# Kernel optimization log

Measured on AMD Instinct MI355X. Metric: run time of the kernel, lower is better.

## Reference

```python
import jax, jax.numpy as jnp
import numpy as np

DIM = 256; SEQ = 2048; WIN = 64; HEADS = 4; RANK = 32; LAYERS = 3; VOCAB = 32000
EPS = 1e-6

def _unit(v):
    # unit_normalize_values: project onto unit sphere along feature dim
    return v / jnp.maximum(jnp.linalg.norm(v, axis=-1, keepdims=True), EPS)

def _signed_softmax(s):
    # signed_softmax_state: sign(s) * softmax(|s|) over nodes
    return jnp.sign(s) * jax.nn.softmax(jnp.abs(s), axis=-1)

def setup_inputs() -> dict:
    key = jax.random.key(0)
    ks = jax.random.split(key, 10)
    d = DIM
    return {
        "input_ids": jax.random.randint(ks[0], (2, SEQ), 0, VOCAB, dtype=jnp.int32),
        "emb": 0.02 * jax.random.normal(ks[1], (VOCAB, d), jnp.float32),
        "pos_emb": 0.02 * jax.random.normal(ks[2], (SEQ, d), jnp.float32),
        "anchor_val": 0.02 * jax.random.normal(ks[3], (d,), jnp.float32),
        "anchor_state": jnp.zeros((), jnp.float32),
        "Ws": 0.02 * jax.random.normal(ks[4], (d,), jnp.float32),
        "bs": jnp.zeros((), jnp.float32),
        "U": 0.02 * jax.random.normal(ks[5], (LAYERS, d, HEADS, RANK), jnp.float32),
        "V": 0.02 * jax.random.normal(ks[6], (LAYERS, d, HEADS, RANK), jnp.float32),
        "W1": 0.02 * jax.random.normal(ks[7], (LAYERS, d, 2 * d), jnp.float32),
        "b1": jnp.zeros((LAYERS, 2 * d), jnp.float32),
        "W2": 0.02 * jax.random.normal(ks[8], (LAYERS, 2 * d, d), jnp.float32),
        "b2": jnp.zeros((LAYERS, d), jnp.float32),
    }

def _forward(emb, pos_emb, anchor_val, anchor_state, Ws, bs, U, V, W1, b1, W2, b2, input_ids):
    B, S = input_ids.shape
    tok = emb[input_ids] + pos_emb[None, :S]          # [B,S,D]
    state_src = tok                                    # state projected from pre-unit-norm values
    tok = _unit(tok)
    tstate = state_src @ Ws + bs                       # [B,S] scalar state per node
    val = jnp.concatenate([jnp.broadcast_to(_unit(anchor_val), (B, 1, DIM)), tok], axis=1)
    state = jnp.concatenate([jnp.broadcast_to(anchor_state, (B, 1)), tstate], axis=1)
    N = S + 1
    offs = jnp.arange(-WIN, WIN + 1)
    idx = jnp.arange(N)[:, None] + offs[None, :]       # [N,K]
    valid = (idx >= 0) & (idx < N)
    idxc = jnp.clip(idx, 0, N - 1)
    inv_sqrt_r = np.float32(1.0 / np.sqrt(RANK))
    for l in range(LAYERS):
        q = jnp.einsum('bnd,dhr->bnhr', val, U[l])
        k = jnp.einsum('bnd,dhr->bnhr', val, V[l])
        knb = k[:, idxc]                               # [B,N,K,H,R] window gather
        s = jnp.einsum('bnhr,bnkhr->bnkh', q, knb) * inv_sqrt_r
        s = s.max(axis=-1)                             # max head-aggregate [B,N,K]
        a = jnp.where(valid, jnp.abs(s), -jnp.inf)
        wgt = jnp.where(valid, jnp.sign(s) * jax.nn.softmax(a, axis=-1), 0.0)  # signed-abs-softmax edges
        dval = jnp.einsum('bnk,bnkd->bnd', wgt, val[:, idxc])
        dstate = jnp.sum(wgt * state[:, idxc], axis=-1)
        # apply_delta: residual + norm(identity) + unit-norm + touched-mask where
        updated = val + dval
        nv = _unit(updated)
        touched = jnp.max(jnp.abs(jax.lax.stop_gradient(dval)), axis=-1, keepdims=True) > 0
        val = jnp.where(touched, nv, updated)
        state = _signed_softmax(state + dstate)
        # residual feed-forward then re-unit-norm
        h = jax.nn.gelu(jnp.einsum('bnd,dh->bnh', val, W1[l]) + b1[l], approximate=False)
        val = _unit(val + jnp.einsum('bnh,hd->bnd', h, W2[l]) + b2[l])
    return state, val

def reference(input_ids, emb, pos_emb, anchor_val, anchor_state, Ws, bs, U, V, W1, b1, W2, b2):
    return _forward(emb, pos_emb, anchor_val, anchor_state, Ws, bs, U, V, W1, b1, W2, b2, input_ids)
```

## Files before the change

### kernel.cpp

```cpp
#include <hip/hip_runtime.h>
#include <hip/hip_bf16.h>
#include <math.h>

#define BB 2
#define SS 2048
#define NN 2049
#define MM (BB*NN)
#define DD 256
#define HR 128
#define NHEAD 4
#define WINW 64
#define DFF 512
#define EPSF 1e-6f
#define TB8 257

typedef __attribute__((ext_vector_type(8))) short bf16x8;
typedef __attribute__((ext_vector_type(4))) float f32x4;

__device__ __forceinline__ float wave_sum(float v) {
    v += __shfl_down(v, 32, 64); v += __shfl_down(v, 16, 64);
    v += __shfl_down(v, 8, 64);  v += __shfl_down(v, 4, 64);
    v += __shfl_down(v, 2, 64);  v += __shfl_down(v, 1, 64);
    return v;
}
__device__ __forceinline__ float wave_max(float v) {
    v = fmaxf(v, __shfl_down(v, 32, 64)); v = fmaxf(v, __shfl_down(v, 16, 64));
    v = fmaxf(v, __shfl_down(v, 8, 64));  v = fmaxf(v, __shfl_down(v, 4, 64));
    v = fmaxf(v, __shfl_down(v, 2, 64));  v = fmaxf(v, __shfl_down(v, 1, 64));
    return v;
}
__device__ __forceinline__ float block_sum(float v, float* red) {
    v = wave_sum(v);
    __syncthreads();
    if ((threadIdx.x & 63) == 0) red[threadIdx.x >> 6] = v;
    __syncthreads();
    return red[0] + red[1] + red[2] + red[3];
}
__device__ __forceinline__ float sgnf(float x) {
    return (x > 0.f) ? 1.f : ((x < 0.f) ? -1.f : 0.f);
}
__device__ __forceinline__ ushort f2b(float x) {
    __hip_bfloat16 h = __float2bfloat16(x);
    return *(ushort*)&h;
}
__device__ __forceinline__ float b2f(ushort u) {
    unsigned int v = ((unsigned int)u) << 16;
    return *(float*)&v;
}
__device__ __forceinline__ void split3(float x, ushort& h, ushort& m, ushort& l) {
    h = f2b(x);
    float r1 = x - b2f(h);
    m = f2b(r1);
    l = f2b(r1 - b2f(m));
}
__device__ __forceinline__ void pack_map(int e, int N, int& k, int& n) {
    int j = e & 7;
    int l = (e >> 3) & 63;
    int c = e >> 9;
    int ntiles = N >> 4;
    int kt = c / ntiles, nt = c - kt * ntiles;
    k = kt * 32 + ((l >> 4) << 3) + j;
    n = nt * 16 + (l & 15);
}
__device__ __forceinline__ void dma16(const ushort* g, ushort* lds) {
    __builtin_amdgcn_global_load_lds(
        (const __attribute__((address_space(1))) unsigned int*)g,
        (__attribute__((address_space(3))) unsigned int*)lds,
        16, 0, 0);
}

__global__ void pre_kernel(const int* __restrict__ ids,
                           const float* __restrict__ emb,
                           const float* __restrict__ pos,
                           const float* __restrict__ anchor_val,
                           const float* __restrict__ anchor_state,
                           const float* __restrict__ Ws,
                           const float* __restrict__ bs,
                           float* __restrict__ val,
                           ushort* __restrict__ v0, ushort* __restrict__ v1,
                           ushort* __restrict__ v2,
                           float* __restrict__ state,
                           const float* __restrict__ W1, const float* __restrict__ W2,
                           const float* __restrict__ U,  const float* __restrict__ V,
                           ushort* __restrict__ W1ph, ushort* __restrict__ W1pl,
                           ushort* __restrict__ W2ph, ushort* __restrict__ W2pl,
                           ushort* __restrict__ U0, ushort* __restrict__ U1,
                           ushort* __restrict__ U2,
                           ushort* __restrict__ V0, ushort* __restrict__ V1,
                           ushort* __restrict__ V2) {
    __shared__ float red[4];
    int bid = blockIdx.x;
    int t = threadIdx.x;
    if (bid < MM) {
        int b = bid / NN, n = bid % NN;
        float e;
        if (n == 0) {
            e = anchor_val[t];
        } else {
            int id = ids[b * SS + (n - 1)];
            e = emb[(size_t)id * DD + t] + pos[(size_t)(n - 1) * DD + t];
        }
        float ss = block_sum(e * e, red);
        float ts = block_sum(e * Ws[t], red);
        float rn = 1.f / fmaxf(sqrtf(ss), EPSF);
        float o = e * rn;
        size_t oi = (size_t)bid * DD + t;
        val[oi] = o;
        ushort h, m, lo;
        split3(o, h, m, lo);
        v0[oi] = h; v1[oi] = m; v2[oi] = lo;
        if (t == 0) state[bid] = (n == 0) ? anchor_state[0] : (ts + bs[0]);
        return;
    }
    int idx = (bid - MM) * 256 + t;
    int l = idx / 327680;
    int r = idx - l * 327680;
    if (l >= 3) return;
    int k, n;
    if (r < 131072) {
        int e = r;
        pack_map(e, 512, k, n);
        float s = W1[(size_t)l * 131072 + (size_t)k * 512 + n];
        ushort h = f2b(s);
        W1ph[(size_t)l * 131072 + e] = h;
        W1pl[(size_t)l * 131072 + e] = f2b(s - b2f(h));
    } else if (r < 262144) {
        int e = r - 131072;
        pack_map(e, 256, k, n);
        float s = W2[(size_t)l * 131072 + (size_t)k * 256 + n];
        ushort h = f2b(s);
        W2ph[(size_t)l * 131072 + e] = h;
        W2pl[(size_t)l * 131072 + e] = f2b(s - b2f(h));
    } else if (r < 294912) {
        int e = r - 262144;
        pack_map(e, 128, k, n);
        ushort h, m, lo;
        split3(U[(size_t)l * 32768 + (size_t)k * 128 + n], h, m, lo);
        U0[(size_t)l * 32768 + e] = h;
        U1[(size_t)l * 32768 + e] = m;
        U2[(size_t)l * 32768 + e] = lo;
    } else {
        int e = r - 294912;
        pack_map(e, 128, k, n);
        ushort h, m, lo;
        split3(V[(size_t)l * 32768 + (size_t)k * 128 + n], h, m, lo);
        V0[(size_t)l * 32768 + e] = h;
        V1[(size_t)l * 32768 + e] = m;
        V2[(size_t)l * 32768 + e] = lo;
    }
}

__global__ __launch_bounds__(256, 2)
void proj_kernel(const ushort* __restrict__ X0, const ushort* __restrict__ X1,
                 const ushort* __restrict__ X2,
                 const ushort* __restrict__ U0, const ushort* __restrict__ U1,
                 const ushort* __restrict__ U2,
                 const ushort* __restrict__ V0, const ushort* __restrict__ V1,
                 const ushort* __restrict__ V2,
                 ushort* __restrict__ q0, ushort* __restrict__ q1,
                 ushort* __restrict__ q2,
                 ushort* __restrict__ k0, ushort* __restrict__ k1,
                 ushort* __restrict__ k2) {
    __shared__ __align__(16) ushort stage[2][24 * 512];
    int t = threadIdx.x;
    int w = t >> 6, l = t & 63;
    int lm = l & 15, quad = l >> 4;
    int m0 = blockIdx.x * 16;
    bool isQ = (blockIdx.y == 0);
    const ushort* P[3];
    P[0] = isQ ? U0 : V0;
    P[1] = isQ ? U1 : V1;
    P[2] = isQ ? U2 : V2;
    int row0 = m0 + lm; if (row0 > MM - 1) row0 = MM - 1;
    const ushort* xb0 = X0 + (size_t)row0 * DD + quad * 8;
    const ushort* xb1 = X1 + (size_t)row0 * DD + quad * 8;
    const ushort* xb2 = X2 + (size_t)row0 * DD + quad * 8;

    bf16x8 a0[2], a1[2], a2[2];
    a0[0] = *(const bf16x8*)(xb0);
    a1[0] = *(const bf16x8*)(xb1);
    a2[0] = *(const bf16x8*)(xb2);
    #pragma unroll
    for (int i = 0; i < 6; i++) {
        int c = w * 6 + i;
        int p = c >> 3, ntl = c & 7;
        dma16(P[p] + ((size_t)ntl * 64 + l) * 8,
              &stage[0][c * 512 + l * 8]);
    }
    asm volatile("" ::: "memory");

    f32x4 acc[2];
    acc[0] = (f32x4)(0.f); acc[1] = (f32x4)(0.f);
    #pragma unroll
    for (int kt = 0; kt < 8; kt++) {
        int cur = kt & 1;
        if (kt < 7) {
            a0[cur ^ 1] = *(const bf16x8*)(xb0 + (kt + 1) * 32);
            a1[cur ^ 1] = *(const bf16x8*)(xb1 + (kt + 1) * 32);
            a2[cur ^ 1] = *(const bf16x8*)(xb2 + (kt + 1) * 32);
            #pragma unroll
            for (int i = 0; i < 6; i++) {
                int c = w * 6 + i;
                int p = c >> 3, ntl = c & 7;
                dma16(P[p] + ((size_t)((kt + 1) * 8 + ntl) * 64 + l) * 8,
                      &stage[cur ^ 1][c * 512 + l * 8]);
            }
            asm volatile("s_waitcnt vmcnt(9)" ::: "memory");
        } else {
            asm volatile("s_waitcnt vmcnt(0)" ::: "memory");
        }
        __builtin_amdgcn_s_barrier();
        #pragma unroll
        for (int jj = 0; jj < 2; jj++) {
            int ntl = w * 2 + jj;
            bf16x8 b0 = *(const bf16x8*)&stage[cur][(0 * 8 + ntl) * 512 + l * 8];
            bf16x8 b1 = *(const bf16x8*)&stage[cur][(1 * 8 + ntl) * 512 + l * 8];
            bf16x8 b2 = *(const bf16x8*)&stage[cur][(2 * 8 + ntl) * 512 + l * 8];
            acc[jj] = __builtin_amdgcn_mfma_f32_16x16x32_bf16(a0[cur], b0, acc[jj], 0, 0, 0);
            acc[jj] = __builtin_amdgcn_mfma_f32_16x16x32_bf16(a0[cur], b1, acc[jj], 0, 0, 0);
            acc[jj] = __builtin_amdgcn_mfma_f32_16x16x32_bf16(a1[cur], b0, acc[jj], 0, 0, 0);
            acc[jj] = __builtin_amdgcn_mfma_f32_16x16x32_bf16(a1[cur], b1, acc[jj], 0, 0, 0);
            acc[jj] = __builtin_amdgcn_mfma_f32_16x16x32_bf16(a0[cur], b2, acc[jj], 0, 0, 0);
            acc[jj] = __builtin_amdgcn_mfma_f32_16x16x32_bf16(a2[cur], b0, acc[jj], 0, 0, 0);
        }
        __builtin_amdgcn_s_barrier();
    }
    ushort* o0 = isQ ? q0 : k0;
    ushort* o1 = isQ ? q1 : k1;
    ushort* o2 = isQ ? q2 : k2;
    #pragma unroll
    for (int jj = 0; jj < 2; jj++) {
        int n = (w * 2 + jj) * 16 + lm;
        #pragma unroll
        for (int r = 0; r < 4; r++) {
            int tok = m0 + quad * 4 + r;
            if (tok < MM) {
                ushort h, m, lo;
                split3(acc[jj][r], h, m, lo);
                size_t oi = (size_t)tok * HR + n;
                o0[oi] = h; o1[oi] = m; o2[oi] = lo;
            }
        }
    }
}

__global__ __launch_bounds__(256, 2)
void attn_kernel(const float* __restrict__ val_in,
                 const float* __restrict__ state_in,
                 const ushort* __restrict__ q0, const ushort* __restrict__ q1,
                 const ushort* __restrict__ q2,
                 const ushort* __restrict__ k0, const ushort* __restrict__ k1,
                 const ushort* __restrict__ k2,
                 float* __restrict__ val_out,
                 ushort* __restrict__ vbH, ushort* __restrict__ vbM,
                 float* __restrict__ dstate_out) {
    __shared__ float sc4[NHEAD][8][148];
    __shared__ float wgt2[144][12];
    __shared__ float redS[8][4];
    __shared__ float redM[8][4];

    int b = blockIdx.x / TB8;
    int n0 = (blockIdx.x % TB8) * 8;
    int t = threadIdx.x;
    int w = t >> 6, l = t & 63;
    int lm = l & 15, quad = l >> 4;

    {
        int qrow = n0 + (lm & 7);
        if (qrow > NN - 1) qrow = NN - 1;
        size_t qa = ((size_t)(b * NN + qrow)) * HR + w * 32 + quad * 8;
        bf16x8 a0 = *(const bf16x8*)(q0 + qa);
        bf16x8 a1 = *(const bf16x8*)(q1 + qa);
        bf16x8 a2 = *(const bf16x8*)(q2 + qa);
        bf16x8 kf0[9], kf1[9], kf2[9];
        #pragma unroll
        for (int jt = 0; jt < 9; jt++) {
            int j = n0 - 64 + jt * 16 + lm;
            j = (j < 0) ? 0 : ((j > NN - 1) ? NN - 1 : j);
            size_t ka = ((size_t)(b * NN + j)) * HR + w * 32 + quad * 8;
            kf0[jt] = *(const bf16x8*)(k0 + ka);
            kf1[jt] = *(const bf16x8*)(k1 + ka);
            kf2[jt] = *(const bf16x8*)(k2 + ka);
        }
        #pragma unroll
        for (int jt = 0; jt < 9; jt++) {
            f32x4 acc = (f32x4)(0.f);
            acc = __builtin_amdgcn_mfma_f32_16x16x32_bf16(a0, kf0[jt], acc, 0, 0, 0);
            acc = __builtin_amdgcn_mfma_f32_16x16x32_bf16(a0, kf1[jt], acc, 0, 0, 0);
            acc = __builtin_amdgcn_mfma_f32_16x16x32_bf16(a1, kf0[jt], acc, 0, 0, 0);
            acc = __builtin_amdgcn_mfma_f32_16x16x32_bf16(a1, kf1[jt], acc, 0, 0, 0);
            acc = __builtin_amdgcn_mfma_f32_16x16x32_bf16(a0, kf2[jt], acc, 0, 0, 0);
            acc = __builtin_amdgcn_mfma_f32_16x16x32_bf16(a2, kf0[jt], acc, 0, 0, 0);
            if (quad < 2) {
                #pragma unroll
                for (int r = 0; r < 4; r++)
                    sc4[w][quad * 4 + r][jt * 16 + lm] = acc[r];
            }
        }
    }
    __syncthreads();

    {
        int m = t >> 5, p = t & 31;
        int n = n0 + m;
        bool tokv = (n < NN);
        float sv[5]; bool vv[5];
        float mx = -INFINITY;
        #pragma unroll
        for (int i = 0; i < 5; i++) {
            int tap = p + 32 * i;
            bool inb = (tap < 144);
            int tapc = inb ? tap : 0;
            int j = n0 - 64 + tapc;
            float s0 = sc4[0][m][tapc], s1 = sc4[1][m][tapc];
            float s2 = sc4[2][m][tapc], s3 = sc4[3][m][tapc];
            float s = fmaxf(fmaxf(s0, s1), fmaxf(s2, s3)) * 0.17677669529663687f;
            bool v = inb && tokv && (tap >= m) && (tap <= m + 128) && (j >= 0) && (j < NN);
            sv[i] = s; vv[i] = v;
            if (v) mx = fmaxf(mx, fabsf(s));
        }
        for (int off = 16; off > 0; off >>= 1) mx = fmaxf(mx, __shfl_xor(mx, off, 64));
        float ee[5];
        float sum = 0.f;
        #pragma unroll
        for (int i = 0; i < 5; i++) {
            ee[i] = vv[i] ? expf(fabsf(sv[i]) - mx) : 0.f;
            sum += ee[i];
        }
        for (int off = 16; off > 0; off >>= 1) sum += __shfl_xor(sum, off, 64);
        float inv = (sum > 0.f) ? 1.f / sum : 0.f;
        float ds = 0.f;
        #pragma unroll
        for (int i = 0; i < 5; i++) {
            int tap = p + 32 * i;
            if (tap < 144) {
                float wg = vv[i] ? sgnf(sv[i]) * ee[i] * inv : 0.f;
                wgt2[tap][m] = wg;
                if (vv[i]) ds += wg * state_in[b * NN + (n0 - 64 + tap)];
            }
        }
        for (int off = 16; off > 0; off >>= 1) ds += __shfl_xor(ds, off, 64);
        if (p == 0 && tokv) dstate_out[b * NN + n] = ds;
    }
    __syncthreads();

    {
        int d = (t >> 2) * 4;
        int tg = t & 3;
        int tok0 = tg * 2, tok1 = tg * 2 + 1;
        int jlo = (n0 >= 64) ? 0 : (64 - n0);
        int jhi = NN - 1 - n0 + 64; if (jhi > 135) jhi = 135;
        const float* vbase = val_in + ((size_t)(b * NN + n0 - 64)) * DD + d;
        f32x4 acc0 = (f32x4)(0.f), acc1 = (f32x4)(0.f);
        int jj = jlo;
        for (; jj + 3 <= jhi; jj += 4) {
            f32x4 v0 = *(const f32x4*)(vbase + (size_t)(jj + 0) * DD);
            f32x4 v1 = *(const f32x4*)(vbase + (size_t)(jj + 1) * DD);
            f32x4 v2 = *(const f32x4*)(vbase + (size_t)(jj + 2) * DD);
            f32x4 v3 = *(const f32x4*)(vbase + (size_t)(jj + 3) * DD);
            float wa0 = wgt2[jj + 0][tok0], wa1 = wgt2[jj + 0][tok1];
            float wb0 = wgt2[jj + 1][tok0], wb1 = wgt2[jj + 1][tok1];
            float wc0 = wgt2[jj + 2][tok0], wc1 = wgt2[jj + 2][tok1];
            float wd0 = wgt2[jj + 3][tok0], wd1 = wgt2[jj + 3][tok1];
            #pragma unroll
            for (int c = 0; c < 4; c++) {
                acc0[c] += v0[c] * wa0 + v1[c] * wb0 + v2[c] * wc0 + v3[c] * wd0;
                acc1[c] += v0[c] * wa1 + v1[c] * wb1 + v2[c] * wc1 + v3[c] * wd1;
            }
        }
        for (; jj <= jhi; jj++) {
            f32x4 v = *(const f32x4*)(vbase + (size_t)jj * DD);
            float w0 = wgt2[jj][tok0], w1 = wgt2[jj][tok1];
            #pragma unroll
            for (int c = 0; c < 4; c++) {
                acc0[c] += v[c] * w0;
                acc1[c] += v[c] * w1;
            }
        }
        f32x4 u[2]; f32x4 ac[2]; ac[0] = acc0; ac[1] = acc1;
        #pragma unroll
        for (int ti = 0; ti < 2; ti++) {
            int tok = tg * 2 + ti;
            int n = n0 + tok;
            f32x4 vold = (f32x4)(0.f);
            if (n < NN) vold = *(const f32x4*)(val_in + ((size_t)(b * NN + n)) * DD + d);
            u[ti] = vold + ac[ti];
            float s = u[ti][0]*u[ti][0] + u[ti][1]*u[ti][1] + u[ti][2]*u[ti][2] + u[ti][3]*u[ti][3];
            float mb = fmaxf(fmaxf(fabsf(ac[ti][0]), fabsf(ac[ti][1])),
                             fmaxf(fabsf(ac[ti][2]), fabsf(ac[ti][3])));
            for (int off = 4; off <= 32; off <<= 1) {
                s += __shfl_xor(s, off, 64);
                mb = fmaxf(mb, __shfl_xor(mb, off, 64));
            }
            if ((l >> 2) == 0) { redS[tok][w] = s; redM[tok][w] = mb; }
        }
        __syncthreads();
        #pragma unroll
        for (int ti = 0; ti < 2; ti++) {
            int tok = tg * 2 + ti;
            int n = n0 + tok;
            if (n < NN) {
                float ss = redS[tok][0] + redS[tok][1] + redS[tok][2] + redS[tok][3];
                float mab = fmaxf(fmaxf(redM[tok][0], redM[tok][1]),
                                  fmaxf(redM[tok][2], redM[tok][3]));
                float rn = 1.f / fmaxf(sqrtf(ss), EPSF);
                f32x4 o = u[ti];
                if (mab > 0.f) { o[0] *= rn; o[1] *= rn; o[2] *= rn; o[3] *= rn; }
                size_t oi = ((size_t)(b * NN + n)) * DD + d;
                *(f32x4*)(val_out + oi) = o;
                ushort4 hv, mv;
                {
                    ushort h0 = f2b(o[0]); hv.x = h0; mv.x = f2b(o[0] - b2f(h0));
                    ushort h1 = f2b(o[1]); hv.y = h1; mv.y = f2b(o[1] - b2f(h1));
                    ushort h2 = f2b(o[2]); hv.z = h2; mv.z = f2b(o[2] - b2f(h2));
                    ushort h3 = f2b(o[3]); hv.w = h3; mv.w = f2b(o[3] - b2f(h3));
                }
                *(ushort4*)(vbH + oi) = hv;
                *(ushort4*)(vbM + oi) = mv;
            }
        }
    }
}

__global__ __launch_bounds__(256, 2)
void ffn1_kernel(const ushort* __restrict__ XbH, const ushort* __restrict__ XbM,
                 const ushort* __restrict__ W1h, const ushort* __restrict__ W1l,
                 const float*  __restrict__ b1,
                 ushort* __restrict__ Hh, ushort* __restrict__ Hl,
                 const float* __restrict__ state_in, const float* __restrict__ dstate,
                 float* __restrict__ state_out) {
    __shared__ __align__(16) ushort stage[2][32 * 512];
    int t = threadIdx.x;

    if (blockIdx.x == 257) {
        float* red = (float*)&stage[0][0];
        int b = blockIdx.y;
        float lmax = -INFINITY;
        for (int n = t; n < NN; n += 256) {
            float x = state_in[b * NN + n] + dstate[b * NN + n];
            lmax = fmaxf(lmax, fabsf(x));
        }
        lmax = wave_max(lmax);
        if ((t & 63) == 0) red[t >> 6] = lmax;
        __syncthreads();
        float m = fmaxf(fmaxf(red[0], red[1]), fmaxf(red[2], red[3]));
        float lsum = 0.f;
        for (int n = t; n < NN; n += 256)
            lsum += expf(fabsf(state_in[b * NN + n] + dstate[b * NN + n]) - m);
        lsum = wave_sum(lsum);
        __syncthreads();
        if ((t & 63) == 0) red[4 + (t >> 6)] = lsum;
        __syncthreads();
        float inv = 1.f / (red[4] + red[5] + red[6] + red[7]);
        for (int n = t; n < NN; n += 256) {
            float x = state_in[b * NN + n] + dstate[b * NN + n];
            state_out[b * NN + n] = sgnf(x) * expf(fabsf(x) - m) * inv;
        }
        return;
    }

    int w = t >> 6, l = t & 63;
    int lm = l & 15, quad = l >> 4;
    int m0 = blockIdx.x * 16;
    int nh = blockIdx.y;
    int row0 = m0 + lm; if (row0 > MM - 1) row0 = MM - 1;
    const ushort* xh = XbH + (size_t)row0 * DD + quad * 8;
    const ushort* xm = XbM + (size_t)row0 * DD + quad * 8;

    bf16x8 ah[2], am[2];
    ah[0] = *(const bf16x8*)(xh);
    am[0] = *(const bf16x8*)(xm);
    #pragma unroll
    for (int i = 0; i < 8; i++) {
        int c = w * 8 + i;
        int p = c >> 4, ntl = c & 15;
        const ushort* src = (p ? W1l : W1h) + ((size_t)(nh * 16 + ntl) * 64 + l) * 8;
        dma16(src, &stage[0][c * 512 + l * 8]);
    }
    asm volatile("" ::: "memory");

    f32x4 acc[4];
    #pragma unroll
    for (int jj = 0; jj < 4; jj++) acc[jj] = (f32x4)(0.f);

    #pragma unroll
    for (int kt = 0; kt < 8; kt++) {
        int cur = kt & 1;
        if (kt < 7) {
            ah[cur ^ 1] = *(const bf16x8*)(xh + (kt + 1) * 32);
            am[cur ^ 1] = *(const bf16x8*)(xm + (kt + 1) * 32);
            #pragma unroll
            for (int i = 0; i < 8; i++) {
                int c = w * 8 + i;
                int p = c >> 4, ntl = c & 15;
                const ushort* src = (p ? W1l : W1h) +
                    ((size_t)((kt + 1) * 32 + nh * 16 + ntl) * 64 + l) * 8;
                dma16(src, &stage[cur ^ 1][c * 512 + l * 8]);
            }
            asm volatile("s_waitcnt vmcnt(10)" ::: "memory");
        } else {
            asm volatile("s_waitcnt vmcnt(0)" ::: "memory");
        }
        __builtin_amdgcn_s_barrier();
        #pragma unroll
        for (int jj = 0; jj < 4; jj++) {
            int ntl = w * 4 + jj;
            bf16x8 bh = *(const bf16x8*)&stage[cur][ntl * 512 + l * 8];
            bf16x8 bl = *(const bf16x8*)&stage[cur][(16 + ntl) * 512 + l * 8];
            acc[jj] = __builtin_amdgcn_mfma_f32_16x16x32_bf16(ah[cur], bh, acc[jj], 0, 0, 0);
            acc[jj] = __builtin_amdgcn_mfma_f32_16x16x32_bf16(am[cur], bh, acc[jj], 0, 0, 0);
            acc[jj] = __builtin_amdgcn_mfma_f32_16x16x32_bf16(ah[cur], bl, acc[jj], 0, 0, 0);
        }
        __builtin_amdgcn_s_barrier();
    }
    #pragma unroll
    for (int jj = 0; jj < 4; jj++) {
        int gn = nh * 256 + (w * 4 + jj) * 16 + lm;
        float bb = b1[gn];
        #pragma unroll
        for (int r = 0; r < 4; r++) {
            int tok = m0 + quad * 4 + r;
            if (tok < MM) {
                float x = acc[jj][r] + bb;
                float g = 0.5f * x * (1.f + erff(x * 0.70710678118654752f));
                ushort gh = f2b(g);
                size_t oi = (size_t)tok * DFF + gn;
                Hh[oi] = gh;
                Hl[oi] = f2b(g - b2f(gh));
            }
        }
    }
}

__global__ __launch_bounds__(256, 2)
void ffn2_kernel(const ushort* __restrict__ Hh, const ushort* __restrict__ Hl,
                 const float*  __restrict__ Xf,
                 const ushort* __restrict__ W2h, const ushort* __restrict__ W2l,
                 const float*  __restrict__ b2,
                 float* __restrict__ Yb) {
    __shared__ __align__(16) ushort stage[2][16 * 512];
    int t = threadIdx.x;
    int w = t >> 6, l = t & 63;
    int lm = l & 15, quad = l >> 4;
    int m0 = blockIdx.x * 16;
    int nh = blockIdx.y;
    int row0 = m0 + lm; if (row0 > MM - 1) row0 = MM - 1;
    const ushort* xh = Hh + (size_t)row0 * DFF + quad * 8;
    const ushort* xl = Hl + (size_t)row0 * DFF + quad * 8;

    bf16x8 ah[2], al[2];
    ah[0] = *(const bf16x8*)(xh);
    al[0] = *(const bf16x8*)(xl);
    #pragma unroll
    for (int i = 0; i < 4; i++) {
        int c = w * 4 + i;
        int p = c >> 3, ntl = c & 7;
        const ushort* src = (p ? W2l : W2h) + ((size_t)(nh * 8 + ntl) * 64 + l) * 8;
        dma16(src, &stage[0][c * 512 + l * 8]);
    }
    asm volatile("" ::: "memory");

    f32x4 acc[2];
    acc[0] = (f32x4)(0.f); acc[1] = (f32x4)(0.f);

    #pragma unroll
    for (int kt = 0; kt < 16; kt++) {
        int cur = kt & 1;
        if (kt < 15) {
            ah[cur ^ 1] = *(const bf16x8*)(xh + (kt + 1) * 32);
            al[cur ^ 1] = *(const bf16x8*)(xl + (kt + 1) * 32);
            #pragma unroll
            for (int i = 0; i < 4; i++) {
                int c = w * 4 + i;
                int p = c >> 3, ntl = c & 7;
                const ushort* src = (p ? W2l : W2h) +
                    ((size_t)((kt + 1) * 16 + nh * 8 + ntl) * 64 + l) * 8;
                dma16(src, &stage[cur ^ 1][c * 512 + l * 8]);
            }
            asm volatile("s_waitcnt vmcnt(6)" ::: "memory");
        } else {
            asm volatile("s_waitcnt vmcnt(0)" ::: "memory");
        }
        __builtin_amdgcn_s_barrier();
        #pragma unroll
        for (int jj = 0; jj < 2; jj++) {
            int ntl = w * 2 + jj;
            bf16x8 bh = *(const bf16x8*)&stage[cur][ntl * 512 + l * 8];
            bf16x8 bl = *(const bf16x8*)&stage[cur][(8 + ntl) * 512 + l * 8];
            acc[jj] = __builtin_amdgcn_mfma_f32_16x16x32_bf16(ah[cur], bh, acc[jj], 0, 0, 0);
            acc[jj] = __builtin_amdgcn_mfma_f32_16x16x32_bf16(al[cur], bh, acc[jj], 0, 0, 0);
            acc[jj] = __builtin_amdgcn_mfma_f32_16x16x32_bf16(ah[cur], bl, acc[jj], 0, 0, 0);
        }
        __builtin_amdgcn_s_barrier();
    }
    #pragma unroll
    for (int jj = 0; jj < 2; jj++) {
        int gn = nh * 128 + (w * 2 + jj) * 16 + lm;
        float bb = b2[gn];
        #pragma unroll
        for (int r = 0; r < 4; r++) {
            int tok = m0 + quad * 4 + r;
            if (tok < MM) {
                size_t oi = (size_t)tok * DD + gn;
                Yb[oi] = Xf[oi] + acc[jj][r] + bb;
            }
        }
    }
}

__global__ void ffn3_kernel(const float* __restrict__ Yb,
                            float* __restrict__ val_out,
                            ushort* __restrict__ o0, ushort* __restrict__ o1,
                            ushort* __restrict__ o2) {
    int t = threadIdx.x;
    int w = t >> 6, l = t & 63;
    int row = blockIdx.x * 4 + w;
    if (row >= MM) return;
    f32x4 y = *(const f32x4*)(Yb + (size_t)row * DD + l * 4);
    float s = y[0]*y[0] + y[1]*y[1] + y[2]*y[2] + y[3]*y[3];
    #pragma unroll
    for (int off = 1; off < 64; off <<= 1) s += __shfl_xor(s, off, 64);
    float rn = 1.f / fmaxf(sqrtf(s), EPSF);
    f32x4 o;
    o[0] = y[0] * rn; o[1] = y[1] * rn; o[2] = y[2] * rn; o[3] = y[3] * rn;
    size_t oi = (size_t)row * DD + l * 4;
    *(f32x4*)(val_out + oi) = o;
    ushort4 h4, m4, l4;
    ushort hh, mm, ll;
    split3(o[0], hh, mm, ll); h4.x = hh; m4.x = mm; l4.x = ll;
    split3(o[1], hh, mm, ll); h4.y = hh; m4.y = mm; l4.y = ll;
    split3(o[2], hh, mm, ll); h4.z = hh; m4.z = mm; l4.z = ll;
    split3(o[3], hh, mm, ll); h4.w = hh; m4.w = mm; l4.w = ll;
    *(ushort4*)(o0 + oi) = h4;
    *(ushort4*)(o1 + oi) = m4;
    *(ushort4*)(o2 + oi) = l4;
}

extern "C" void kernel_launch(void* const* d_in, const int* in_sizes, int n_in,
                              void* d_out, int out_size, void* d_ws, size_t ws_size,
                              hipStream_t stream) {
    const int*   ids          = (const int*)d_in[0];
    const float* emb          = (const float*)d_in[1];
    const float* pos          = (const float*)d_in[2];
    const float* anchor_val   = (const float*)d_in[3];
    const float* anchor_state = (const float*)d_in[4];
    const float* Ws           = (const float*)d_in[5];
    const float* bs           = (const float*)d_in[6];
    const float* U            = (const float*)d_in[7];
    const float* V            = (const float*)d_in[8];
    const float* W1           = (const float*)d_in[9];
    const float* b1           = (const float*)d_in[10];
    const float* W2           = (const float*)d_in[11];
    const float* b2           = (const float*)d_in[12];
    float* out = (float*)d_out;

    ushort* p = (ushort*)d_ws;
    ushort* vA0 = p; p += (size_t)MM * DD;
    ushort* vA1 = p; p += (size_t)MM * DD;
    ushort* vA2 = p; p += (size_t)MM * DD;
    ushort* vB0 = p; p += (size_t)MM * DD;
    ushort* vB1 = p; p += (size_t)MM * DD;
    ushort* q0b = p; p += (size_t)MM * HR;
    ushort* q1b = p; p += (size_t)MM * HR;
    ushort* q2b = p; p += (size_t)MM * HR;
    ushort* k0b = p; p += (size_t)MM * HR;
    ushort* k1b = p; p += (size_t)MM * HR;
    ushort* k2b = p; p += (size_t)MM * HR;
    ushort* Hh  = p; p += (size_t)MM * DFF;
    ushort* Hl  = p; p += (size_t)MM * DFF;
    ushort* W1ph = p; p += 3 * 131072;
    ushort* W1pl = p; p += 3 * 131072;
    ushort* W2ph = p; p += 3 * 131072;
    ushort* W2pl = p; p += 3 * 131072;
    ushort* U0p = p; p += 3 * 32768;
    ushort* U1p = p; p += 3 * 32768;
    ushort* U2p = p; p += 3 * 32768;
    ushort* V0p = p; p += 3 * 32768;
    ushort* V1p = p; p += 3 * 32768;
    ushort* V2p = p; p += 3 * 32768;
    float* f = (float*)p;
    float* valA = f; f += (size_t)MM * DD;
    float* valB = f; f += (size_t)MM * DD;
    float* st0  = f; f += MM;
    float* st1  = f; f += MM;
    float* dst  = f; f += MM;
    float* Yb   = valA;

    pre_kernel<<<MM + 3840, 256, 0, stream>>>(ids, emb, pos, anchor_val, anchor_state,
                                              Ws, bs, valA, vA0, vA1, vA2, st0,
                                              W1, W2, U, V,
                                              W1ph, W1pl, W2ph, W2pl,
                                              U0p, U1p, U2p, V0p, V1p, V2p);
    float* s_in = st0;
    float* s_out = st1;
    for (int l = 0; l < 3; l++) {
        proj_kernel<<<dim3(257, 2), 256, 0, stream>>>(
            vA0, vA1, vA2,
            U0p + (size_t)l * 32768, U1p + (size_t)l * 32768, U2p + (size_t)l * 32768,
            V0p + (size_t)l * 32768, V1p + (size_t)l * 32768, V2p + (size_t)l * 32768,
            q0b, q1b, q2b, k0b, k1b, k2b);
        attn_kernel<<<BB * TB8, 256, 0, stream>>>(valA, s_in,
                                                  q0b, q1b, q2b, k0b, k1b, k2b,
                                                  valB, vB0, vB1, dst);
        ffn1_kernel<<<dim3(258, 2), 256, 0, stream>>>(
            vB0, vB1,
            W1ph + (size_t)l * 131072, W1pl + (size_t)l * 131072, b1 + (size_t)l * DFF,
            Hh, Hl,
            s_in, dst, (l == 2) ? out : s_out);
        ffn2_kernel<<<dim3(257, 2), 256, 0, stream>>>(
            Hh, Hl, valB,
            W2ph + (size_t)l * 131072, W2pl + (size_t)l * 131072, b2 + (size_t)l * DD,
            Yb);
        ffn3_kernel<<<(MM + 3) / 4, 256, 0, stream>>>(
            Yb, (l == 2) ? (out + MM) : valA, vA0, vA1, vA2);
        float* tmp = s_in; s_in = s_out; s_out = tmp;
    }
}
```

Measured before the change: 357.8 us.

## Fuse final unit-norm and bf16 split into projection kernel, drop ffn3 launches

The per-layer ffn3 kernel, which normalized the FFN output and wrote three bf16 split planes, is removed. The projection kernel now reads fp32 values directly, optionally unit-normalizes each row, writes the normalized fp32 value back (Q blocks only), and builds the three bf16 planes in a swizzled LDS buffer for the MFMA loop. Only the last layer runs a standalone normalization kernel. This saves two kernel launches and the global round trip of the split planes, at the cost of more LDS and duplicated normalization work across the Q and K blocks.

```diff
diff --git a/kernel.cpp b/kernel.cpp
--- a/kernel.cpp
+++ b/kernel.cpp
@@ -77,8 +77,6 @@
                            const float* __restrict__ Ws,
                            const float* __restrict__ bs,
                            float* __restrict__ val,
-                           ushort* __restrict__ v0, ushort* __restrict__ v1,
-                           ushort* __restrict__ v2,
                            float* __restrict__ state,
                            const float* __restrict__ W1, const float* __restrict__ W2,
                            const float* __restrict__ U,  const float* __restrict__ V,
@@ -104,11 +102,7 @@
         float ts = block_sum(e * Ws[t], red);
         float rn = 1.f / fmaxf(sqrtf(ss), EPSF);
         float o = e * rn;
-        size_t oi = (size_t)bid * DD + t;
-        val[oi] = o;
-        ushort h, m, lo;
-        split3(o, h, m, lo);
-        v0[oi] = h; v1[oi] = m; v2[oi] = lo;
+        val[(size_t)bid * DD + t] = o;
         if (t == 0) state[bid] = (n == 0) ? anchor_state[0] : (ts + bs[0]);
         return;
     }
@@ -151,8 +145,7 @@
 }
 
 __global__ __launch_bounds__(256, 2)
-void proj_kernel(const ushort* __restrict__ X0, const ushort* __restrict__ X1,
-                 const ushort* __restrict__ X2,
+void proj_kernel(const float* __restrict__ Xin,
                  const ushort* __restrict__ U0, const ushort* __restrict__ U1,
                  const ushort* __restrict__ U2,
                  const ushort* __restrict__ V0, const ushort* __restrict__ V1,
@@ -160,8 +153,10 @@
                  ushort* __restrict__ q0, ushort* __restrict__ q1,
                  ushort* __restrict__ q2,
                  ushort* __restrict__ k0, ushort* __restrict__ k1,
-                 ushort* __restrict__ k2) {
+                 ushort* __restrict__ k2,
+                 float* __restrict__ valG, int donorm) {
     __shared__ __align__(16) ushort stage[2][24 * 512];
+    __shared__ __align__(16) ushort pln[3][16 * 256];
     int t = threadIdx.x;
     int w = t >> 6, l = t & 63;
     int lm = l & 15, quad = l >> 4;
@@ -171,15 +166,7 @@
     P[0] = isQ ? U0 : V0;
     P[1] = isQ ? U1 : V1;
     P[2] = isQ ? U2 : V2;
-    int row0 = m0 + lm; if (row0 > MM - 1) row0 = MM - 1;
-    const ushort* xb0 = X0 + (size_t)row0 * DD + quad * 8;
-    const ushort* xb1 = X1 + (size_t)row0 * DD + quad * 8;
-    const ushort* xb2 = X2 + (size_t)row0 * DD + quad * 8;
-
-    bf16x8 a0[2], a1[2], a2[2];
-    a0[0] = *(const bf16x8*)(xb0);
-    a1[0] = *(const bf16x8*)(xb1);
-    a2[0] = *(const bf16x8*)(xb2);
+
     #pragma unroll
     for (int i = 0; i < 6; i++) {
         int c = w * 6 + i;
@@ -189,15 +176,38 @@
     }
     asm volatile("" ::: "memory");
 
+    #pragma unroll
+    for (int rr = 0; rr < 4; rr++) {
+        int row = w * 4 + rr;
+        int tok = m0 + row; if (tok > MM - 1) tok = MM - 1;
+        f32x4 x = *(const f32x4*)(Xin + (size_t)tok * DD + l * 4);
+        if (donorm) {
+            float s = x[0]*x[0] + x[1]*x[1] + x[2]*x[2] + x[3]*x[3];
+            #pragma unroll
+            for (int off = 1; off < 64; off <<= 1) s += __shfl_xor(s, off, 64);
+            float rn = 1.f / fmaxf(sqrtf(s), EPSF);
+            x[0] *= rn; x[1] *= rn; x[2] *= rn; x[3] *= rn;
+            if (isQ) *(f32x4*)(valG + (size_t)tok * DD + l * 4) = x;
+        }
+        ushort4 h4, m4, l4;
+        ushort hh, mm, ll;
+        split3(x[0], hh, mm, ll); h4.x = hh; m4.x = mm; l4.x = ll;
+        split3(x[1], hh, mm, ll); h4.y = hh; m4.y = mm; l4.y = ll;
+        split3(x[2], hh, mm, ll); h4.z = hh; m4.z = mm; l4.z = ll;
+        split3(x[3], hh, mm, ll); h4.w = hh; m4.w = mm; l4.w = ll;
+        unsigned byte = ((unsigned)(row * 512 + l * 8)) ^ ((unsigned)((row & 7) << 4));
+        *(ushort4*)((char*)&pln[0][0] + byte) = h4;
+        *(ushort4*)((char*)&pln[1][0] + byte) = m4;
+        *(ushort4*)((char*)&pln[2][0] + byte) = l4;
+    }
+    __syncthreads();
+
     f32x4 acc[2];
     acc[0] = (f32x4)(0.f); acc[1] = (f32x4)(0.f);
     #pragma unroll
     for (int kt = 0; kt < 8; kt++) {
         int cur = kt & 1;
         if (kt < 7) {
-            a0[cur ^ 1] = *(const bf16x8*)(xb0 + (kt + 1) * 32);
-            a1[cur ^ 1] = *(const bf16x8*)(xb1 + (kt + 1) * 32);
-            a2[cur ^ 1] = *(const bf16x8*)(xb2 + (kt + 1) * 32);
             #pragma unroll
             for (int i = 0; i < 6; i++) {
                 int c = w * 6 + i;
@@ -205,23 +215,28 @@
                 dma16(P[p] + ((size_t)((kt + 1) * 8 + ntl) * 64 + l) * 8,
                       &stage[cur ^ 1][c * 512 + l * 8]);
             }
-            asm volatile("s_waitcnt vmcnt(9)" ::: "memory");
+            asm volatile("s_waitcnt vmcnt(6)" ::: "memory");
         } else {
             asm volatile("s_waitcnt vmcnt(0)" ::: "memory");
         }
         __builtin_amdgcn_s_barrier();
+        unsigned abyte = ((unsigned)(lm * 512 + kt * 64 + quad * 16)) ^
+                         ((unsigned)((lm & 7) << 4));
+        bf16x8 a0 = *(const bf16x8*)((char*)&pln[0][0] + abyte);
+        bf16x8 a1 = *(const bf16x8*)((char*)&pln[1][0] + abyte);
+        bf16x8 a2 = *(const bf16x8*)((char*)&pln[2][0] + abyte);
         #pragma unroll
         for (int jj = 0; jj < 2; jj++) {
             int ntl = w * 2 + jj;
             bf16x8 b0 = *(const bf16x8*)&stage[cur][(0 * 8 + ntl) * 512 + l * 8];
             bf16x8 b1 = *(const bf16x8*)&stage[cur][(1 * 8 + ntl) * 512 + l * 8];
             bf16x8 b2 = *(const bf16x8*)&stage[cur][(2 * 8 + ntl) * 512 + l * 8];
-            acc[jj] = __builtin_amdgcn_mfma_f32_16x16x32_bf16(a0[cur], b0, acc[jj], 0, 0, 0);
-            acc[jj] = __builtin_amdgcn_mfma_f32_16x16x32_bf16(a0[cur], b1, acc[jj], 0, 0, 0);
-            acc[jj] = __builtin_amdgcn_mfma_f32_16x16x32_bf16(a1[cur], b0, acc[jj], 0, 0, 0);
-            acc[jj] = __builtin_amdgcn_mfma_f32_16x16x32_bf16(a1[cur], b1, acc[jj], 0, 0, 0);
-            acc[jj] = __builtin_amdgcn_mfma_f32_16x16x32_bf16(a0[cur], b2, acc[jj], 0, 0, 0);
-            acc[jj] = __builtin_amdgcn_mfma_f32_16x16x32_bf16(a2[cur], b0, acc[jj], 0, 0, 0);
+            acc[jj] = __builtin_amdgcn_mfma_f32_16x16x32_bf16(a0, b0, acc[jj], 0, 0, 0);
+            acc[jj] = __builtin_amdgcn_mfma_f32_16x16x32_bf16(a0, b1, acc[jj], 0, 0, 0);
+            acc[jj] = __builtin_amdgcn_mfma_f32_16x16x32_bf16(a1, b0, acc[jj], 0, 0, 0);
+            acc[jj] = __builtin_amdgcn_mfma_f32_16x16x32_bf16(a1, b1, acc[jj], 0, 0, 0);
+            acc[jj] = __builtin_amdgcn_mfma_f32_16x16x32_bf16(a0, b2, acc[jj], 0, 0, 0);
+            acc[jj] = __builtin_amdgcn_mfma_f32_16x16x32_bf16(a2, b0, acc[jj], 0, 0, 0);
         }
         __builtin_amdgcn_s_barrier();
     }
@@ -608,10 +623,8 @@
     }
 }
 
-__global__ void ffn3_kernel(const float* __restrict__ Yb,
-                            float* __restrict__ val_out,
-                            ushort* __restrict__ o0, ushort* __restrict__ o1,
-                            ushort* __restrict__ o2) {
+__global__ void ffn3f_kernel(const float* __restrict__ Yb,
+                             float* __restrict__ val_out) {
     int t = threadIdx.x;
     int w = t >> 6, l = t & 63;
     int row = blockIdx.x * 4 + w;
@@ -623,17 +636,7 @@
     float rn = 1.f / fmaxf(sqrtf(s), EPSF);
     f32x4 o;
     o[0] = y[0] * rn; o[1] = y[1] * rn; o[2] = y[2] * rn; o[3] = y[3] * rn;
-    size_t oi = (size_t)row * DD + l * 4;
-    *(f32x4*)(val_out + oi) = o;
-    ushort4 h4, m4, l4;
-    ushort hh, mm, ll;
-    split3(o[0], hh, mm, ll); h4.x = hh; m4.x = mm; l4.x = ll;
-    split3(o[1], hh, mm, ll); h4.y = hh; m4.y = mm; l4.y = ll;
-    split3(o[2], hh, mm, ll); h4.z = hh; m4.z = mm; l4.z = ll;
-    split3(o[3], hh, mm, ll); h4.w = hh; m4.w = mm; l4.w = ll;
-    *(ushort4*)(o0 + oi) = h4;
-    *(ushort4*)(o1 + oi) = m4;
-    *(ushort4*)(o2 + oi) = l4;
+    *(f32x4*)(val_out + (size_t)row * DD + l * 4) = o;
 }
 
 extern "C" void kernel_launch(void* const* d_in, const int* in_sizes, int n_in,
@@ -655,9 +658,6 @@
     float* out = (float*)d_out;
 
     ushort* p = (ushort*)d_ws;
-    ushort* vA0 = p; p += (size_t)MM * DD;
-    ushort* vA1 = p; p += (size_t)MM * DD;
-    ushort* vA2 = p; p += (size_t)MM * DD;
     ushort* vB0 = p; p += (size_t)MM * DD;
     ushort* vB1 = p; p += (size_t)MM * DD;
     ushort* q0b = p; p += (size_t)MM * HR;
@@ -681,24 +681,26 @@
     float* f = (float*)p;
     float* valA = f; f += (size_t)MM * DD;
     float* valB = f; f += (size_t)MM * DD;
+    float* Yb   = f; f += (size_t)MM * DD;
     float* st0  = f; f += MM;
     float* st1  = f; f += MM;
     float* dst  = f; f += MM;
-    float* Yb   = valA;
 
     pre_kernel<<<MM + 3840, 256, 0, stream>>>(ids, emb, pos, anchor_val, anchor_state,
-                                              Ws, bs, valA, vA0, vA1, vA2, st0,
+                                              Ws, bs, valA, st0,
                                               W1, W2, U, V,
                                               W1ph, W1pl, W2ph, W2pl,
                                               U0p, U1p, U2p, V0p, V1p, V2p);
     float* s_in = st0;
     float* s_out = st1;
     for (int l = 0; l < 3; l++) {
+        const float* Xin = (l == 0) ? valA : Yb;
         proj_kernel<<<dim3(257, 2), 256, 0, stream>>>(
-            vA0, vA1, vA2,
+            Xin,
             U0p + (size_t)l * 32768, U1p + (size_t)l * 32768, U2p + (size_t)l * 32768,
             V0p + (size_t)l * 32768, V1p + (size_t)l * 32768, V2p + (size_t)l * 32768,
-            q0b, q1b, q2b, k0b, k1b, k2b);
+            q0b, q1b, q2b, k0b, k1b, k2b,
+            valA, (l == 0) ? 0 : 1);
         attn_kernel<<<BB * TB8, 256, 0, stream>>>(valA, s_in,
                                                   q0b, q1b, q2b, k0b, k1b, k2b,
                                                   valB, vB0, vB1, dst);
@@ -711,8 +713,7 @@
             Hh, Hl, valB,
             W2ph + (size_t)l * 131072, W2pl + (size_t)l * 131072, b2 + (size_t)l * DD,
             Yb);
-        ffn3_kernel<<<(MM + 3) / 4, 256, 0, stream>>>(
-            Yb, (l == 2) ? (out + MM) : valA, vA0, vA1, vA2);
         float* tmp = s_in; s_in = s_out; s_out = tmp;
     }
-}
+    ffn3f_kernel<<<(MM + 3) / 4, 256, 0, stream>>>(Yb, out + MM);
+}
```

Result: no change. 351.3 us (-1.8%).
